# Kernel optimization log

Hardware: AMD Instinct MI355X
Metric: run time of the kernel (lower is better)

The kernel has to match this reference:

```python
import jax, jax.numpy as jnp
import numpy as np

N_SYS = 64      # number of systems
N_ELEC = 64     # electrons per system
DIM = 256
HEADS = 8
EPS = 1e-6      # flax LayerNorm default epsilon


def _edge_indices():
    # all intra-system electron pairs (including self), block-diagonal structure
    ii, jj = np.meshgrid(np.arange(N_ELEC), np.arange(N_ELEC), indexing='ij')
    offs = (np.arange(N_SYS) * N_ELEC)[:, None, None]
    ei = (offs + ii[None]).reshape(-1).astype(np.int32)
    ej = (offs + jj[None]).reshape(-1).astype(np.int32)
    return jnp.asarray(ei), jnp.asarray(ej)


def setup_inputs() -> dict:
    key = jax.random.key(0)
    ks = jax.random.split(key, 8)
    n = N_SYS * N_ELEC
    ei, ej = _edge_indices()
    s = 1.0 / np.sqrt(DIM)
    return {
        'h_one': jax.random.normal(ks[0], (n, DIM), jnp.float32),
        'W_qkv': jax.random.normal(ks[1], (DIM, 3 * DIM), jnp.float32) * s,
        'W_out': jax.random.normal(ks[2], (DIM, DIM), jnp.float32) * s,
        'ln1_scale': jnp.ones((DIM,), jnp.float32),
        'ln1_bias': jnp.zeros((DIM,), jnp.float32),
        'W_mlp': jax.random.normal(ks[3], (DIM, DIM), jnp.float32) * s,
        'b_mlp': jnp.zeros((DIM,), jnp.float32),
        'ln2_scale': jnp.ones((DIM,), jnp.float32),
        'ln2_bias': jnp.zeros((DIM,), jnp.float32),
        'e_e_i': ei,
        'e_e_j': ej,
    }


def _layernorm(x, scale, bias):
    mu = jnp.mean(x, axis=-1, keepdims=True)
    var = jnp.mean(jnp.square(x - mu), axis=-1, keepdims=True)
    return (x - mu) * jax.lax.rsqrt(var + EPS) * scale + bias


def _segment_softmax(logits, seg, n):
    mx = jax.ops.segment_max(logits, seg, num_segments=n)
    e = jnp.exp(logits - mx[seg])
    denom = jax.ops.segment_sum(e, seg, num_segments=n)
    return e / denom[seg]


def reference(h_one, W_qkv, W_out, ln1_scale, ln1_bias, W_mlp, b_mlp,
              ln2_scale, ln2_bias, e_e_i, e_e_j):
    n = h_one.shape[0]
    hd = DIM // HEADS
    qkv = h_one @ W_qkv                                  # [n, 3*dim]
    Q, K, V = jnp.split(qkv, 3, axis=-1)
    Q = Q.reshape(n, HEADS, hd)
    K = K.reshape(n, HEADS, hd)
    V = V.reshape(n, HEADS, hd)
    # per-edge attention scores: Q[i] . K[j] over head dim -> [E, H]
    A = jnp.einsum('ehd,ehd->eh', Q[e_e_i], K[e_e_j]) / jnp.sqrt(jnp.float32(hd))
    # NOTE: softmax segmented by e_e_j, scatter-sum by e_e_i (faithful to source)
    A = _segment_softmax(A, e_e_j, n)
    attn = jax.ops.segment_sum(A[..., None] * V[e_e_j], e_e_i, num_segments=n)
    attn = attn.reshape(n, DIM)
    h = h_one + attn @ W_out
    h = _layernorm(h, ln1_scale, ln1_bias)
    h = h + jax.nn.silu(h @ W_mlp + b_mlp)
    h = _layernorm(h, ln2_scale, ln2_bias)
    return h
```

## Files before the change

### kernel.cpp

```cpp
#include <hip/hip_runtime.h>
#include <hip/hip_bf16.h>
#include <math.h>

#define N_SYS   64
#define N_ELEC  64
#define NTOT    (N_SYS * N_ELEC)
#define DIM     256
#define HEADS   8
#define LN_EPS  1e-6f

typedef __attribute__((ext_vector_type(8))) short bf16x8;
typedef __attribute__((ext_vector_type(4))) short short4v;
typedef __attribute__((ext_vector_type(4))) float f32x4;

static __device__ __forceinline__ short f2bf(float f) {
    __hip_bfloat16 h = __float2bfloat16(f);
    return *reinterpret_cast<short*>(&h);
}

__global__ __launch_bounds__(256) void k1_qkv_attn(
    const float* __restrict__ h_one, const float* __restrict__ W_qkv,
    const float* __restrict__ Wout, const float* __restrict__ Wmlp,
    short* __restrict__ attn, short* __restrict__ WoutT,
    short* __restrict__ WmlpT)
{
    const int tid = threadIdx.x;

    if (blockIdx.x >= 512) {
        const int b2 = blockIdx.x - 512;
        const float* src = (b2 < 16) ? Wout : Wmlp;
        short* dst = (b2 < 16) ? WoutT : WmlpT;
        const int tile = b2 & 15;
        const int tk = (tile >> 2) * 64, tn = (tile & 3) * 64;
#pragma unroll
        for (int p = 0; p < 4; ++p) {
            int idx = p * 256 + tid;
            int kk = idx >> 4, n4 = (idx & 15) * 4;
            float4 v = *(const float4*)&src[(size_t)(tk + kk) * 256 + tn + n4];
            dst[(size_t)(tn + n4 + 0) * 256 + tk + kk] = f2bf(v.x);
            dst[(size_t)(tn + n4 + 1) * 256 + tk + kk] = f2bf(v.y);
            dst[(size_t)(tn + n4 + 2) * 256 + tk + kk] = f2bf(v.z);
            dst[(size_t)(tn + n4 + 3) * 256 + tk + kk] = f2bf(v.w);
        }
        return;
    }

    const int s = blockIdx.x & 63;
    const int h = blockIdx.x >> 6;

    __shared__ short Ha[64][72];
    __shared__ short Bs[96][72];
    __shared__ short Qs[64][40];
    __shared__ short Ks[64][40];
    __shared__ short Vt[32][72];
    __shared__ short Pm[64][72];

    const int lane = tid & 63;
    const int w = tid >> 6;
    const int l15 = lane & 15;
    const int l4 = lane >> 4;

    const float* Abase = h_one + (size_t)s * 64 * 256;
    const int rA = tid >> 3;
    const int cA8 = (tid & 7) * 8;
    const int bkk = tid >> 2;
    const int btt = tid & 3;

    float4 ra[2][4];
    float4 rb[2][6];

#define K1_LOAD(buf, kbase)                                                        \
    do {                                                                           \
        const float* ap0 = &Abase[(size_t)rA * 256 + (kbase) + cA8];               \
        const float* ap1 = &Abase[(size_t)(rA + 32) * 256 + (kbase) + cA8];        \
        ra[buf][0] = *(const float4*)ap0;                                          \
        ra[buf][1] = *(const float4*)(ap0 + 4);                                    \
        ra[buf][2] = *(const float4*)ap1;                                          \
        ra[buf][3] = *(const float4*)(ap1 + 4);                                    \
        _Pragma("unroll")                                                          \
        for (int q = 0; q < 6; ++q) {                                              \
            int c = btt + q * 4;                                                   \
            int g = c >> 3;                                                        \
            int c4 = (c & 7) * 4;                                                  \
            rb[buf][q] = *(const float4*)&W_qkv[(size_t)((kbase) + bkk) * 768      \
                                                + g * 256 + h * 32 + c4];          \
        }                                                                          \
    } while (0)

    f32x4 acc[6] = {};

    K1_LOAD(0, 0);

#pragma unroll
    for (int kk = 0; kk < 4; ++kk) {
        const int k0 = kk * 64;
        const int cur = kk & 1;
        const int nxt = cur ^ 1;

        if (kk) __syncthreads();
        {
            bf16x8 o;
            o[0] = f2bf(ra[cur][0].x); o[1] = f2bf(ra[cur][0].y);
            o[2] = f2bf(ra[cur][0].z); o[3] = f2bf(ra[cur][0].w);
            o[4] = f2bf(ra[cur][1].x); o[5] = f2bf(ra[cur][1].y);
            o[6] = f2bf(ra[cur][1].z); o[7] = f2bf(ra[cur][1].w);
            *(bf16x8*)&Ha[rA][cA8] = o;
            o[0] = f2bf(ra[cur][2].x); o[1] = f2bf(ra[cur][2].y);
            o[2] = f2bf(ra[cur][2].z); o[3] = f2bf(ra[cur][2].w);
            o[4] = f2bf(ra[cur][3].x); o[5] = f2bf(ra[cur][3].y);
            o[6] = f2bf(ra[cur][3].z); o[7] = f2bf(ra[cur][3].w);
            *(bf16x8*)&Ha[rA + 32][cA8] = o;
        }
#pragma unroll
        for (int q = 0; q < 6; ++q) {
            int c = btt + q * 4;
            int g = c >> 3;
            int c4 = (c & 7) * 4;
            Bs[g * 32 + c4 + 0][bkk] = f2bf(rb[cur][q].x);
            Bs[g * 32 + c4 + 1][bkk] = f2bf(rb[cur][q].y);
            Bs[g * 32 + c4 + 2][bkk] = f2bf(rb[cur][q].z);
            Bs[g * 32 + c4 + 3][bkk] = f2bf(rb[cur][q].w);
        }
        if (kk < 3) K1_LOAD(nxt, k0 + 64);
        __syncthreads();

#pragma unroll
        for (int ki = 0; ki < 2; ++ki) {
            bf16x8 af = *(const bf16x8*)&Ha[w * 16 + l15][ki * 32 + l4 * 8];
#pragma unroll
            for (int nf = 0; nf < 6; ++nf) {
                bf16x8 bfv = *(const bf16x8*)&Bs[nf * 16 + l15][ki * 32 + l4 * 8];
                acc[nf] = __builtin_amdgcn_mfma_f32_16x16x32_bf16(af, bfv, acc[nf], 0, 0, 0);
            }
        }
    }
#undef K1_LOAD

#pragma unroll
    for (int nf = 0; nf < 6; ++nf) {
        int c = nf * 16 + l15;
#pragma unroll
        for (int j = 0; j < 4; ++j) {
            int row = w * 16 + l4 * 4 + j;
            short v = f2bf(acc[nf][j]);
            if (c < 32)       Qs[row][c] = v;
            else if (c < 64)  Ks[row][c - 32] = v;
            else              Vt[c - 64][row] = v;
        }
    }
    __syncthreads();

    const float scale = 0.17677669529663687f;
    f32x4 sacc[4] = {};
    {
        bf16x8 ak = *(const bf16x8*)&Ks[w * 16 + l15][l4 * 8];
#pragma unroll
        for (int nf = 0; nf < 4; ++nf) {
            bf16x8 bq = *(const bf16x8*)&Qs[nf * 16 + l15][l4 * 8];
            sacc[nf] = __builtin_amdgcn_mfma_f32_16x16x32_bf16(ak, bq, sacc[nf], 0, 0, 0);
        }
    }
#pragma unroll
    for (int nf = 0; nf < 4; ++nf) sacc[nf] *= scale;
#pragma unroll
    for (int jj = 0; jj < 4; ++jj) {
        float mx = fmaxf(fmaxf(sacc[0][jj], sacc[1][jj]),
                         fmaxf(sacc[2][jj], sacc[3][jj]));
        mx = fmaxf(mx, __shfl_xor(mx, 1, 64));
        mx = fmaxf(mx, __shfl_xor(mx, 2, 64));
        mx = fmaxf(mx, __shfl_xor(mx, 4, 64));
        mx = fmaxf(mx, __shfl_xor(mx, 8, 64));
        float e0 = __expf(sacc[0][jj] - mx);
        float e1 = __expf(sacc[1][jj] - mx);
        float e2 = __expf(sacc[2][jj] - mx);
        float e3 = __expf(sacc[3][jj] - mx);
        float ss = e0 + e1 + e2 + e3;
        ss += __shfl_xor(ss, 1, 64);
        ss += __shfl_xor(ss, 2, 64);
        ss += __shfl_xor(ss, 4, 64);
        ss += __shfl_xor(ss, 8, 64);
        float inv = 1.0f / ss;
        sacc[0][jj] = e0 * inv; sacc[1][jj] = e1 * inv;
        sacc[2][jj] = e2 * inv; sacc[3][jj] = e3 * inv;
    }
#pragma unroll
    for (int nf = 0; nf < 4; ++nf) {
        short4v pq;
        pq[0] = f2bf(sacc[nf][0]); pq[1] = f2bf(sacc[nf][1]);
        pq[2] = f2bf(sacc[nf][2]); pq[3] = f2bf(sacc[nf][3]);
        *(short4v*)&Pm[nf * 16 + l15][w * 16 + l4 * 4] = pq;
    }
    __syncthreads();

    f32x4 pv[2] = {};
#pragma unroll
    for (int ki = 0; ki < 2; ++ki) {
        bf16x8 ap = *(const bf16x8*)&Pm[w * 16 + l15][ki * 32 + l4 * 8];
#pragma unroll
        for (int nf = 0; nf < 2; ++nf) {
            bf16x8 bv = *(const bf16x8*)&Vt[nf * 16 + l15][ki * 32 + l4 * 8];
            pv[nf] = __builtin_amdgcn_mfma_f32_16x16x32_bf16(ap, bv, pv[nf], 0, 0, 0);
        }
    }
#pragma unroll
    for (int nf = 0; nf < 2; ++nf)
#pragma unroll
        for (int j = 0; j < 4; ++j)
            attn[(size_t)(s * 64 + w * 16 + l4 * 4 + j) * 256 + h * 32 + nf * 16 + l15]
                = f2bf(pv[nf][j]);
}

__global__ __launch_bounds__(512) void k2_tail(
    const short* __restrict__ attnbf, const short* __restrict__ WoutT,
    const short* __restrict__ WmlpT, const float* __restrict__ h_one,
    const float* __restrict__ b_mlp,
    const float* __restrict__ ln1_s, const float* __restrict__ ln1_b,
    const float* __restrict__ ln2_s, const float* __restrict__ ln2_b,
    float* __restrict__ out)
{
    const int r0 = blockIdx.x * 16;

    __shared__ short Abf[16][264];
    __shared__ float H1[16][260];
    __shared__ short L1[16][264];

    const int tid = threadIdx.x;
    const int lane = tid & 63;
    const int w = tid >> 6;
    const int l15 = lane & 15;
    const int l4 = lane >> 4;

    const size_t wrow0 = (size_t)(w * 32 + l15) * 256;
    const size_t wrow1 = (size_t)(w * 32 + 16 + l15) * 256;

    {
        int r = tid >> 5, c8 = (tid & 31) * 8;
        *(bf16x8*)&Abf[r][c8] = *(const bf16x8*)&attnbf[(size_t)(r0 + r) * 256 + c8];
    }
    __syncthreads();

    f32x4 acc[2] = {};
    {
        bf16x8 bcur0 = *(const bf16x8*)&WoutT[wrow0 + l4 * 8];
        bf16x8 bcur1 = *(const bf16x8*)&WoutT[wrow1 + l4 * 8];
#pragma unroll
        for (int k0 = 0; k0 < 256; k0 += 32) {
            bf16x8 bnxt0, bnxt1;
            if (k0 < 224) {
                bnxt0 = *(const bf16x8*)&WoutT[wrow0 + k0 + 32 + l4 * 8];
                bnxt1 = *(const bf16x8*)&WoutT[wrow1 + k0 + 32 + l4 * 8];
            }
            bf16x8 af = *(const bf16x8*)&Abf[l15][k0 + l4 * 8];
            acc[0] = __builtin_amdgcn_mfma_f32_16x16x32_bf16(af, bcur0, acc[0], 0, 0, 0);
            acc[1] = __builtin_amdgcn_mfma_f32_16x16x32_bf16(af, bcur1, acc[1], 0, 0, 0);
            bcur0 = bnxt0; bcur1 = bnxt1;
        }
    }
#pragma unroll
    for (int nf = 0; nf < 2; ++nf) {
        int col = w * 32 + nf * 16 + l15;
#pragma unroll
        for (int j = 0; j < 4; ++j) {
            int row = l4 * 4 + j;
            H1[row][col] = acc[nf][j] + h_one[(size_t)(r0 + row) * 256 + col];
        }
    }
    __syncthreads();

    {
        float4 sc = *(const float4*)&ln1_s[lane * 4];
        float4 bi = *(const float4*)&ln1_b[lane * 4];
#pragma unroll
        for (int rr = 0; rr < 2; ++rr) {
            int row = w * 2 + rr;
            float4 v = *(const float4*)&H1[row][lane * 4];
            float su = v.x + v.y + v.z + v.w;
#pragma unroll
            for (int off = 32; off > 0; off >>= 1) su += __shfl_xor(su, off, 64);
            float mu = su * (1.0f / 256.0f);
            float dx = v.x - mu, dy = v.y - mu, dz = v.z - mu, dw = v.w - mu;
            float s2 = dx * dx + dy * dy + dz * dz + dw * dw;
#pragma unroll
            for (int off = 32; off > 0; off >>= 1) s2 += __shfl_xor(s2, off, 64);
            float inv = rsqrtf(s2 * (1.0f / 256.0f) + LN_EPS);
            float4 o;
            o.x = dx * inv * sc.x + bi.x;
            o.y = dy * inv * sc.y + bi.y;
            o.z = dz * inv * sc.z + bi.z;
            o.w = dw * inv * sc.w + bi.w;
            *(float4*)&H1[row][lane * 4] = o;
            short4v ob;
            ob[0] = f2bf(o.x); ob[1] = f2bf(o.y); ob[2] = f2bf(o.z); ob[3] = f2bf(o.w);
            *(short4v*)&L1[row][lane * 4] = ob;
        }
    }
    __syncthreads();

    f32x4 acc2[2] = {};
    {
        bf16x8 bcur0 = *(const bf16x8*)&WmlpT[wrow0 + l4 * 8];
        bf16x8 bcur1 = *(const bf16x8*)&WmlpT[wrow1 + l4 * 8];
#pragma unroll
        for (int k0 = 0; k0 < 256; k0 += 32) {
            bf16x8 bnxt0, bnxt1;
            if (k0 < 224) {
                bnxt0 = *(const bf16x8*)&WmlpT[wrow0 + k0 + 32 + l4 * 8];
                bnxt1 = *(const bf16x8*)&WmlpT[wrow1 + k0 + 32 + l4 * 8];
            }
            bf16x8 af = *(const bf16x8*)&L1[l15][k0 + l4 * 8];
            acc2[0] = __builtin_amdgcn_mfma_f32_16x16x32_bf16(af, bcur0, acc2[0], 0, 0, 0);
            acc2[1] = __builtin_amdgcn_mfma_f32_16x16x32_bf16(af, bcur1, acc2[1], 0, 0, 0);
            bcur0 = bnxt0; bcur1 = bnxt1;
        }
    }
#pragma unroll
    for (int nf = 0; nf < 2; ++nf) {
        int col = w * 32 + nf * 16 + l15;
        float bm = b_mlp[col];
#pragma unroll
        for (int j = 0; j < 4; ++j) {
            int row = l4 * 4 + j;
            float v = acc2[nf][j] + bm;
            float sg = 1.0f / (1.0f + __expf(-v));
            H1[row][col] = H1[row][col] + v * sg;
        }
    }
    __syncthreads();

    {
        float4 sc = *(const float4*)&ln2_s[lane * 4];
        float4 bi = *(const float4*)&ln2_b[lane * 4];
#pragma unroll
        for (int rr = 0; rr < 2; ++rr) {
            int row = w * 2 + rr;
            float4 v = *(const float4*)&H1[row][lane * 4];
            float su = v.x + v.y + v.z + v.w;
#pragma unroll
            for (int off = 32; off > 0; off >>= 1) su += __shfl_xor(su, off, 64);
            float mu = su * (1.0f / 256.0f);
            float dx = v.x - mu, dy = v.y - mu, dz = v.z - mu, dw = v.w - mu;
            float s2 = dx * dx + dy * dy + dz * dz + dw * dw;
#pragma unroll
            for (int off = 32; off > 0; off >>= 1) s2 += __shfl_xor(s2, off, 64);
            float inv = rsqrtf(s2 * (1.0f / 256.0f) + LN_EPS);
            float4 o;
            o.x = dx * inv * sc.x + bi.x;
            o.y = dy * inv * sc.y + bi.y;
            o.z = dz * inv * sc.z + bi.z;
            o.w = dw * inv * sc.w + bi.w;
            *(float4*)&out[(size_t)(r0 + row) * 256 + lane * 4] = o;
        }
    }
}

extern "C" void kernel_launch(void* const* d_in, const int* in_sizes, int n_in,
                              void* d_out, int out_size, void* d_ws, size_t ws_size,
                              hipStream_t stream)
{
    const float* h_one = (const float*)d_in[0];
    const float* W_qkv = (const float*)d_in[1];
    const float* W_out = (const float*)d_in[2];
    const float* ln1_s = (const float*)d_in[3];
    const float* ln1_b = (const float*)d_in[4];
    const float* W_mlp = (const float*)d_in[5];
    const float* b_mlp = (const float*)d_in[6];
    const float* ln2_s = (const float*)d_in[7];
    const float* ln2_b = (const float*)d_in[8];
    float* out = (float*)d_out;

    char* ws = (char*)d_ws;
    short* attn_bf = (short*)ws;
    short* WoutT   = (short*)(ws + 2097152);
    short* WmlpT   = WoutT + 256 * 256;

    k1_qkv_attn<<<544, 256, 0, stream>>>(h_one, W_qkv, W_out, W_mlp,
                                         attn_bf, WoutT, WmlpT);
    k2_tail<<<256, 512, 0, stream>>>(attn_bf, WoutT, WmlpT, h_one, b_mlp,
                                     ln1_s, ln1_b, ln2_s, ln2_b, out);
}
```

Measured before the change: 25.97 us.

## Load A fragments directly into registers and double-buffer B tile in LDS

Each lane now loads the h_one values it needs for its MFMA A-operand straight from global memory and converts them to bf16 in registers, removing the Ha LDS staging buffer. The B tile becomes double-buffered in shared memory, so the barrier at the top of each k-iteration is dropped and one sync per step remains. The cost is less coalesced global loads for A (each row is read by lanes at strided offsets) and more LDS for the second B buffer.

```diff
diff --git a/kernel.cpp b/kernel.cpp
--- a/kernel.cpp
+++ b/kernel.cpp
@@ -48,8 +48,7 @@
     const int s = blockIdx.x & 63;
     const int h = blockIdx.x >> 6;
 
-    __shared__ short Ha[64][72];
-    __shared__ short Bs[96][72];
+    __shared__ short Bs[2][96][72];
     __shared__ short Qs[64][40];
     __shared__ short Ks[64][40];
     __shared__ short Vt[32][72];
@@ -60,9 +59,7 @@
     const int l15 = lane & 15;
     const int l4 = lane >> 4;
 
-    const float* Abase = h_one + (size_t)s * 64 * 256;
-    const int rA = tid >> 3;
-    const int cA8 = (tid & 7) * 8;
+    const float* Arow = h_one + ((size_t)s * 64 + w * 16 + l15) * 256;
     const int bkk = tid >> 2;
     const int btt = tid & 3;
 
@@ -71,12 +68,11 @@
 
 #define K1_LOAD(buf, kbase)                                                        \
     do {                                                                           \
-        const float* ap0 = &Abase[(size_t)rA * 256 + (kbase) + cA8];               \
-        const float* ap1 = &Abase[(size_t)(rA + 32) * 256 + (kbase) + cA8];        \
-        ra[buf][0] = *(const float4*)ap0;                                          \
-        ra[buf][1] = *(const float4*)(ap0 + 4);                                    \
-        ra[buf][2] = *(const float4*)ap1;                                          \
-        ra[buf][3] = *(const float4*)(ap1 + 4);                                    \
+        const float* ap = Arow + (kbase) + l4 * 8;                                 \
+        ra[buf][0] = *(const float4*)ap;                                           \
+        ra[buf][1] = *(const float4*)(ap + 4);                                     \
+        ra[buf][2] = *(const float4*)(ap + 32);                                    \
+        ra[buf][3] = *(const float4*)(ap + 36);                                    \
         _Pragma("unroll")                                                          \
         for (int q = 0; q < 6; ++q) {                                              \
             int c = btt + q * 4;                                                   \
@@ -95,41 +91,30 @@
     for (int kk = 0; kk < 4; ++kk) {
         const int k0 = kk * 64;
         const int cur = kk & 1;
-        const int nxt = cur ^ 1;
-
-        if (kk) __syncthreads();
-        {
-            bf16x8 o;
-            o[0] = f2bf(ra[cur][0].x); o[1] = f2bf(ra[cur][0].y);
-            o[2] = f2bf(ra[cur][0].z); o[3] = f2bf(ra[cur][0].w);
-            o[4] = f2bf(ra[cur][1].x); o[5] = f2bf(ra[cur][1].y);
-            o[6] = f2bf(ra[cur][1].z); o[7] = f2bf(ra[cur][1].w);
-            *(bf16x8*)&Ha[rA][cA8] = o;
-            o[0] = f2bf(ra[cur][2].x); o[1] = f2bf(ra[cur][2].y);
-            o[2] = f2bf(ra[cur][2].z); o[3] = f2bf(ra[cur][2].w);
-            o[4] = f2bf(ra[cur][3].x); o[5] = f2bf(ra[cur][3].y);
-            o[6] = f2bf(ra[cur][3].z); o[7] = f2bf(ra[cur][3].w);
-            *(bf16x8*)&Ha[rA + 32][cA8] = o;
-        }
+
 #pragma unroll
         for (int q = 0; q < 6; ++q) {
             int c = btt + q * 4;
             int g = c >> 3;
             int c4 = (c & 7) * 4;
-            Bs[g * 32 + c4 + 0][bkk] = f2bf(rb[cur][q].x);
-            Bs[g * 32 + c4 + 1][bkk] = f2bf(rb[cur][q].y);
-            Bs[g * 32 + c4 + 2][bkk] = f2bf(rb[cur][q].z);
-            Bs[g * 32 + c4 + 3][bkk] = f2bf(rb[cur][q].w);
-        }
-        if (kk < 3) K1_LOAD(nxt, k0 + 64);
+            Bs[cur][g * 32 + c4 + 0][bkk] = f2bf(rb[cur][q].x);
+            Bs[cur][g * 32 + c4 + 1][bkk] = f2bf(rb[cur][q].y);
+            Bs[cur][g * 32 + c4 + 2][bkk] = f2bf(rb[cur][q].z);
+            Bs[cur][g * 32 + c4 + 3][bkk] = f2bf(rb[cur][q].w);
+        }
+        if (kk < 3) K1_LOAD(cur ^ 1, k0 + 64);
         __syncthreads();
 
 #pragma unroll
         for (int ki = 0; ki < 2; ++ki) {
-            bf16x8 af = *(const bf16x8*)&Ha[w * 16 + l15][ki * 32 + l4 * 8];
+            bf16x8 af;
+            af[0] = f2bf(ra[cur][ki * 2].x);     af[1] = f2bf(ra[cur][ki * 2].y);
+            af[2] = f2bf(ra[cur][ki * 2].z);     af[3] = f2bf(ra[cur][ki * 2].w);
+            af[4] = f2bf(ra[cur][ki * 2 + 1].x); af[5] = f2bf(ra[cur][ki * 2 + 1].y);
+            af[6] = f2bf(ra[cur][ki * 2 + 1].z); af[7] = f2bf(ra[cur][ki * 2 + 1].w);
 #pragma unroll
             for (int nf = 0; nf < 6; ++nf) {
-                bf16x8 bfv = *(const bf16x8*)&Bs[nf * 16 + l15][ki * 32 + l4 * 8];
+                bf16x8 bfv = *(const bf16x8*)&Bs[cur][nf * 16 + l15][ki * 32 + l4 * 8];
                 acc[nf] = __builtin_amdgcn_mfma_f32_16x16x32_bf16(af, bfv, acc[nf], 0, 0, 0);
             }
         }
```

New measurement: 26.92 us. +3.7%, slower.
